# Performance work log

Hardware: AMD Instinct MI355X
Metric: run time of the kernel (lower is better)

The kernel has to match this reference:

```python
import jax, jax.numpy as jnp
import numpy as np

SCALE, K, RADIUS = 4, 32, 0.1
EPS = 1e-5


def fps(p, npoint):
    # Furthest point sampling (CUDA-compatible: starts at index 0). p: (B,N,3) -> (B,npoint) int32
    B, N, _ = p.shape
    d0 = jnp.sum((p - p[:, :1]) ** 2, axis=-1)  # squared dist to point 0, (B,N)

    def step(dist, _):
        nxt = jnp.argmax(dist, axis=-1)                      # (B,)
        lp = p[jnp.arange(B), nxt]                           # (B,3)
        dist = jnp.minimum(dist, jnp.sum((p - lp[:, None]) ** 2, axis=-1))
        return dist, nxt.astype(jnp.int32)

    _, rest = jax.lax.scan(step, d0, None, length=npoint - 1)  # (npoint-1, B)
    idx = jnp.concatenate([jnp.zeros((1, B), jnp.int32), rest], axis=0)
    return idx.T


def ball_query(center, points, radius, k):
    # First-k-by-index neighbors within radius (CUDA ball_query semantics; slots beyond count filled with first hit).
    # center: (B,S,3), points: (B,N,3) -> (B,S,k) int32
    d2 = (jnp.sum(center ** 2, -1)[..., None] + jnp.sum(points ** 2, -1)[:, None, :]
          - 2.0 * jnp.einsum('bsd,bnd->bsn', center, points))  # (B,S,N)
    mask = d2 < radius * radius
    N = points.shape[1]
    score = jnp.where(mask, -jnp.arange(N, dtype=jnp.float32), -jnp.inf)
    vals, idx = jax.lax.top_k(score, k)                      # picks smallest masked indices first
    valid = jnp.isfinite(vals)
    return jnp.where(valid, idx, idx[..., :1])


def convblock(x, w, b, norm=True, act=True):
    # 1x1 conv2d (pointwise) + optional InstanceNorm2d (no affine) + optional ReLU; x: (B,C,S,K)
    x = jnp.einsum('oc,bcsk->bosk', w, x) + b[None, :, None, None]
    if norm:
        m = jnp.mean(x, axis=(2, 3), keepdims=True)
        v = jnp.var(x, axis=(2, 3), keepdims=True)
        x = (x - m) * jax.lax.rsqrt(v + EPS)
    if act:
        x = jax.nn.relu(x)
    return x


def forward(p, f, params):
    B, N, _ = p.shape
    outs_p, outs_f = [p], [f]
    for (w1a, b1a, w1b, b1b, w2a, b2a, w2b, b2b) in params:
        cur_p, cur_f = outs_p[-1], outs_f[-1]
        N = N // SCALE
        idx = fps(cur_p, N)                                          # (B,S)
        center_p = jnp.take_along_axis(cur_p, idx[..., None], axis=1)    # (B,S,3)
        center_f = jnp.take_along_axis(cur_f, idx[:, None, :], axis=2)   # (B,C,S)
        nbr = ball_query(center_p, cur_p, RADIUS, K)                 # (B,S,K)
        gp = jax.vmap(lambda x, i: x[i])(cur_p, nbr)                 # (B,S,K,3)
        dp = jnp.transpose(gp - center_p[:, :, None], (0, 3, 1, 2))  # relative xyz, (B,3,S,K)
        fj = jax.vmap(lambda x, i: x[:, i])(cur_f, nbr)              # (B,C,S,K)
        df = fj - center_f[..., None]                                # 'dp_df' aggregation
        x = jnp.concatenate([dp, df], axis=1)                        # (B,C+3,S,K)
        x = convblock(x, w1a, b1a, norm=True, act=True)
        x = convblock(x, w1b, b1b, norm=False, act=False)
        pooled = jnp.max(x, axis=-1, keepdims=True)
        x = jnp.concatenate([jnp.broadcast_to(pooled, x.shape), x], axis=1)  # (B,2e,S,K)
        x = convblock(x, w2a, b2a, norm=True, act=True)
        x = convblock(x, w2b, b2b, norm=True, act=True)
        outs_f.append(jnp.max(x, axis=-1))                           # (B,e,S)
        outs_p.append(center_p)
    return outs_p, outs_f


def setup_inputs() -> dict:
    key = jax.random.key(0)
    ks = jax.random.split(key, 20)
    B, N = 4, 8192

    def w(k, o, i):
        return jax.random.normal(k, (o, i), jnp.float32) * 0.02

    d = {
        'p': jax.random.uniform(ks[0], (B, N, 3), jnp.float32),
        'f': jax.random.normal(ks[1], (B, 3, N), jnp.float32),
        # stage 1: e=192, c_in=3 -> dp_df channels 6
        'w1_1a': w(ks[2], 192, 6),    'b1_1a': jnp.zeros((192,), jnp.float32),
        'w1_1b': w(ks[3], 192, 192),  'b1_1b': jnp.zeros((192,), jnp.float32),
        'w1_2a': w(ks[4], 384, 384),  'b1_2a': jnp.zeros((384,), jnp.float32),
        'w1_2b': w(ks[5], 192, 384),  'b1_2b': jnp.zeros((192,), jnp.float32),
        # stage 2: e=384, c_in=192 -> dp_df channels 195
        'w2_1a': w(ks[6], 384, 195),  'b2_1a': jnp.zeros((384,), jnp.float32),
        'w2_1b': w(ks[7], 384, 384),  'b2_1b': jnp.zeros((384,), jnp.float32),
        'w2_2a': w(ks[8], 768, 768),  'b2_2a': jnp.zeros((768,), jnp.float32),
        'w2_2b': w(ks[9], 384, 768),  'b2_2b': jnp.zeros((384,), jnp.float32),
    }
    return d


def reference(p, f, w1_1a, b1_1a, w1_1b, b1_1b, w1_2a, b1_2a, w1_2b, b1_2b,
              w2_1a, b2_1a, w2_1b, b2_1b, w2_2a, b2_2a, w2_2b, b2_2b):
    params = [
        (w1_1a, b1_1a, w1_1b, b1_1b, w1_2a, b1_2a, w1_2b, b1_2b),
        (w2_1a, b2_1a, w2_1b, b2_1b, w2_2a, b2_2a, w2_2b, b2_2b),
    ]
    outs_p, outs_f = forward(p, f, params)
    # out_p / out_f lists (excluding the raw inputs, which are passed through unchanged)
    return (outs_p[1], outs_f[1], outs_p[2], outs_f[2])
```

## Files before the change

### kernel.cpp

```cpp
#include <hip/hip_runtime.h>
#include <hip/hip_bf16.h>
#include <hip/hip_fp16.h>
#include <stdint.h>

#define K_NBR 32
#define EPS_F 1e-5f

typedef _Float16 half8v __attribute__((ext_vector_type(8)));
typedef _Float16 half4v __attribute__((ext_vector_type(4)));
typedef float float4v __attribute__((ext_vector_type(4)));

template<int PPT, int MINW>
__global__ __launch_bounds__(256, MINW) void fps_kernel(const float* __restrict__ p, int N, int S,
                                                        int* __restrict__ idx_out,
                                                        float* __restrict__ centers) {
    constexpr int CH = PPT / 4;
    const int b = blockIdx.x;
    const int tid = threadIdx.x;
    const float* pb = p + (size_t)b * N * 3;

    float px[PPT], py[PPT], pz[PPT], dist[PPT];
    const float l0x = pb[0], l0y = pb[1], l0z = pb[2];
#pragma unroll
    for (int j = 0; j < PPT; ++j) {
        int i = j * 256 + tid;
        px[j] = pb[(size_t)i * 3 + 0];
        py[j] = pb[(size_t)i * 3 + 1];
        pz[j] = pb[(size_t)i * 3 + 2];
        float dx = __fsub_rn(px[j], l0x);
        float dy = __fsub_rn(py[j], l0y);
        float dz = __fsub_rn(pz[j], l0z);
        dist[j] = __fadd_rn(__fadd_rn(__fmul_rn(dx, dx), __fmul_rn(dy, dy)), __fmul_rn(dz, dz));
    }

    __shared__ float s_val[2][4];
    __shared__ int   s_idx[2][4];

    if (tid == 0) {
        idx_out[(size_t)b * S] = 0;
        centers[((size_t)b * S) * 3 + 0] = l0x;
        centers[((size_t)b * S) * 3 + 1] = l0y;
        centers[((size_t)b * S) * 3 + 2] = l0z;
    }

    for (int t = 1; t < S; ++t) {
        const int pp = t & 1;
        float v[4]; int ix[4];
#pragma unroll
        for (int k = 0; k < 4; ++k) {
            v[k] = dist[k * CH]; ix[k] = (k * CH) * 256 + tid;
#pragma unroll
            for (int j = 1; j < CH; ++j) {
                if (dist[k * CH + j] > v[k]) { v[k] = dist[k * CH + j]; ix[k] = (k * CH + j) * 256 + tid; }
            }
        }
        float bv = v[0]; int bi = ix[0];
#pragma unroll
        for (int k = 1; k < 4; ++k) if (v[k] > bv) { bv = v[k]; bi = ix[k]; }
#pragma unroll
        for (int off = 32; off >= 1; off >>= 1) {
            float ov = __shfl_down(bv, off);
            int   oi = __shfl_down(bi, off);
            if (ov > bv || (ov == bv && oi < bi)) { bv = ov; bi = oi; }
        }
        if ((tid & 63) == 0) { s_val[pp][tid >> 6] = bv; s_idx[pp][tid >> 6] = bi; }
        __syncthreads();
        bv = s_val[pp][0]; bi = s_idx[pp][0];
#pragma unroll
        for (int w = 1; w < 4; ++w)
            if (s_val[pp][w] > bv || (s_val[pp][w] == bv && s_idx[pp][w] < bi)) { bv = s_val[pp][w]; bi = s_idx[pp][w]; }
        const float lx = pb[(size_t)bi * 3 + 0];
        const float ly = pb[(size_t)bi * 3 + 1];
        const float lz = pb[(size_t)bi * 3 + 2];
        if (tid == 0) {
            idx_out[(size_t)b * S + t] = bi;
            centers[((size_t)b * S + t) * 3 + 0] = lx;
            centers[((size_t)b * S + t) * 3 + 1] = ly;
            centers[((size_t)b * S + t) * 3 + 2] = lz;
        }
#pragma unroll
        for (int j = 0; j < PPT; ++j) {
            float dx = __fsub_rn(px[j], lx);
            float dy = __fsub_rn(py[j], ly);
            float dz = __fsub_rn(pz[j], lz);
            float nd = __fadd_rn(__fadd_rn(__fmul_rn(dx, dx), __fmul_rn(dy, dy)), __fmul_rn(dz, dz));
            dist[j] = fminf(dist[j], nd);
        }
    }
}

__global__ __launch_bounds__(256) void ball_query_kernel(const float* __restrict__ pts,
                                                         const float* __restrict__ ctr,
                                                         int N, int S, int* __restrict__ nbr) {
    int gw   = (int)((blockIdx.x * 256 + threadIdx.x) >> 6);
    int lane = threadIdx.x & 63;
    int b = gw / S;
    int s = gw - b * S;
    const float* pb = pts + (size_t)b * N * 3;
    const float c0 = ctr[((size_t)b * S + s) * 3 + 0];
    const float c1 = ctr[((size_t)b * S + s) * 3 + 1];
    const float c2 = ctr[((size_t)b * S + s) * 3 + 2];
    const float cn = __fadd_rn(__fadd_rn(__fmul_rn(c0, c0), __fmul_rn(c2, c2)), __fmul_rn(c1, c1));
    const float R2 = (float)(0.1 * 0.1);
    int* out = nbr + (size_t)gw * K_NBR;

    int cnt = 0;
    int firstIdx = 0;
    bool haveFirst = false;
    for (int base = 0; base < N && cnt < K_NBR; base += 64) {
        int i = base + lane;
        float x = pb[(size_t)i * 3 + 0];
        float y = pb[(size_t)i * 3 + 1];
        float z = pb[(size_t)i * 3 + 2];
        float pn = __fadd_rn(__fadd_rn(__fmul_rn(x, x), __fmul_rn(z, z)), __fmul_rn(y, y));
        float pr0 = __fmul_rn(c0, x);
        float pr1 = __fmul_rn(c1, y);
        float pr2 = __fmul_rn(c2, z);
        float dt  = __fadd_rn(__fadd_rn(pr0, pr2), pr1);
        float d2 = __fsub_rn(__fadd_rn(cn, pn), __fmul_rn(2.0f, dt));
        bool inR = d2 < R2;
        unsigned long long mask = __ballot(inR);
        if (mask) {
            if (!haveFirst) { haveFirst = true; firstIdx = base + __builtin_ctzll(mask); }
            int rank = __popcll(mask & ((1ull << lane) - 1ull));
            if (inR) {
                int slot = cnt + rank;
                if (slot < K_NBR) out[slot] = i;
            }
            cnt += (int)__popcll(mask);
        }
    }
    if (cnt < K_NBR) {
        for (int sl = cnt + lane; sl < K_NBR; sl += 64) out[sl] = firstIdx;
    }
}

__global__ void gather_cf_kernel(const float* __restrict__ f_b, const int* __restrict__ idx_b,
                                 int N, int S, float* __restrict__ cf, int total) {
    int i = blockIdx.x * 256 + threadIdx.x;
    if (i >= total) return;
    int s = i % S;
    int c = i / S;
    cf[i] = f_b[(size_t)c * N + idx_b[s]];
}

__global__ void build_x_kernel(const float* __restrict__ p_b, const float* __restrict__ f_b,
                               const float* __restrict__ ctr_b, const float* __restrict__ cf,
                               const int* __restrict__ nbr_b,
                               int N, int S, int C, int Cin_pad, int M,
                               _Float16* __restrict__ x) {
    int m = blockIdx.x * 256 + threadIdx.x;
    if (m >= M) return;
    int s = m / K_NBR;
    int n = nbr_b[m];
    const float* pp = p_b + (size_t)n * 3;
    const float* cc = ctr_b + (size_t)s * 3;
    _Float16* row = x + (size_t)m * Cin_pad;
    row[0] = (_Float16)__fsub_rn(pp[0], cc[0]);
    row[1] = (_Float16)__fsub_rn(pp[1], cc[1]);
    row[2] = (_Float16)__fsub_rn(pp[2], cc[2]);
    for (int c = 0; c < C; ++c)
        row[3 + c] = (_Float16)__fsub_rn(f_b[(size_t)c * N + n], cf[(size_t)c * S + s]);
    for (int c = 3 + C; c < Cin_pad; ++c) row[c] = (_Float16)0.f;
}

__global__ void gather_cf2_kernel(const _Float16* __restrict__ ftr, const int* __restrict__ idx_b,
                                  int C, int S, _Float16* __restrict__ cfh, int total) {
    int i = blockIdx.x * 256 + threadIdx.x;
    if (i >= total) return;
    int c = i % C;
    int s = i / C;
    cfh[i] = ftr[(size_t)idx_b[s] * C + c];
}

__global__ void build_x2_kernel(const float* __restrict__ p_b, const _Float16* __restrict__ ftr,
                                const float* __restrict__ ctr_b, const _Float16* __restrict__ cfh,
                                const int* __restrict__ nbr_b,
                                int S, int C, int Cin_pad, int M,
                                _Float16* __restrict__ x) {
    int m = blockIdx.x * 256 + threadIdx.x;
    if (m >= M) return;
    int s = m / K_NBR;
    int n = nbr_b[m];
    const float* pp = p_b + (size_t)n * 3;
    const float* cc = ctr_b + (size_t)s * 3;
    _Float16* row = x + (size_t)m * Cin_pad;
    row[0] = (_Float16)__fsub_rn(pp[0], cc[0]);
    row[1] = (_Float16)__fsub_rn(pp[1], cc[1]);
    row[2] = (_Float16)__fsub_rn(pp[2], cc[2]);
    const _Float16* fr = ftr + (size_t)n * C;
    const _Float16* cr = cfh + (size_t)s * C;
    for (int c = 0; c < C; ++c)
        row[3 + c] = (_Float16)__fsub_rn((float)fr[c], (float)cr[c]);
    for (int c = 3 + C; c < Cin_pad; ++c) row[c] = (_Float16)0.f;
}

__global__ void wconv_kernel(const float* __restrict__ W, int Cin, int Cin_pad,
                             _Float16* __restrict__ Wh, int total) {
    int i = blockIdx.x * 256 + threadIdx.x;
    if (i >= total) return;
    int o = i / Cin_pad, c = i - o * Cin_pad;
    Wh[i] = (c < Cin) ? (_Float16)W[(size_t)o * Cin + c] : (_Float16)0.f;
}

template<bool HAS_POOL, bool NORM_IN, bool STATS>
__global__ __launch_bounds__(256) void conv_mfma_kernel(
    const _Float16* __restrict__ Wh, const float* __restrict__ bias,
    int Cin_pad, int C1,
    const _Float16* __restrict__ Xp,
    const _Float16* __restrict__ X,
    const float* __restrict__ muIn, const float* __restrict__ riIn,
    _Float16* __restrict__ Y,
    int M, int Cout,
    float* __restrict__ psum, float* __restrict__ psq) {
    const int wave = threadIdx.x >> 6;
    const int lane = threadIdx.x & 63;
    const int row  = lane & 15;
    const int kg   = lane >> 4;
    const int m0   = blockIdx.x * 128 + wave * 32;
    const int o0   = blockIdx.y * 64;
    const int mIdx0 = m0 + row;
    const int mIdx1 = m0 + 16 + row;

    float4v acc[2][4];
#pragma unroll
    for (int t = 0; t < 4; ++t) {
        const float* bp = bias + o0 + 16 * t + kg * 4;
        float4v bv4 = (float4v){bp[0], bp[1], bp[2], bp[3]};
        acc[0][t] = bv4;
        acc[1][t] = bv4;
    }
    const int C2 = Cin_pad - C1;
    if (HAS_POOL) {
        const _Float16* pr0 = Xp + (size_t)(mIdx0 >> 5) * C1;
        const _Float16* pr1 = Xp + (size_t)(mIdx1 >> 5) * C1;
        for (int c0 = 0; c0 < C1; c0 += 32) {
            half8v b0 = *(const half8v*)(pr0 + c0 + kg * 8);
            half8v b1 = *(const half8v*)(pr1 + c0 + kg * 8);
#pragma unroll
            for (int t = 0; t < 4; ++t) {
                half8v afr = *(const half8v*)(Wh + (size_t)(o0 + 16 * t + row) * Cin_pad + c0 + kg * 8);
                acc[0][t] = __builtin_amdgcn_mfma_f32_16x16x32_f16(afr, b0, acc[0][t], 0, 0, 0);
                acc[1][t] = __builtin_amdgcn_mfma_f32_16x16x32_f16(afr, b1, acc[1][t], 0, 0, 0);
            }
        }
    }
    const _Float16* xr0 = X + (size_t)mIdx0 * C2;
    const _Float16* xr1 = X + (size_t)mIdx1 * C2;
    for (int c0 = 0; c0 < C2; c0 += 32) {
        half8v b0 = *(const half8v*)(xr0 + c0 + kg * 8);
        half8v b1 = *(const half8v*)(xr1 + c0 + kg * 8);
        if (NORM_IN) {
            const int cb = c0 + kg * 8;
#pragma unroll
            for (int r = 0; r < 8; ++r) {
                float mu = muIn[cb + r], ri = riIn[cb + r];
                b0[r] = (_Float16)fmaxf(((float)b0[r] - mu) * ri, 0.f);
                b1[r] = (_Float16)fmaxf(((float)b1[r] - mu) * ri, 0.f);
            }
        }
#pragma unroll
        for (int t = 0; t < 4; ++t) {
            half8v afr = *(const half8v*)(Wh + (size_t)(o0 + 16 * t + row) * Cin_pad + C1 + c0 + kg * 8);
            acc[0][t] = __builtin_amdgcn_mfma_f32_16x16x32_f16(afr, b0, acc[0][t], 0, 0, 0);
            acc[1][t] = __builtin_amdgcn_mfma_f32_16x16x32_f16(afr, b1, acc[1][t], 0, 0, 0);
        }
    }
#pragma unroll
    for (int w = 0; w < 2; ++w) {
        int mi = (w == 0) ? mIdx0 : mIdx1;
#pragma unroll
        for (int t = 0; t < 4; ++t) {
            half4v hv;
            hv[0] = (_Float16)acc[w][t][0];
            hv[1] = (_Float16)acc[w][t][1];
            hv[2] = (_Float16)acc[w][t][2];
            hv[3] = (_Float16)acc[w][t][3];
            *(half4v*)(Y + (size_t)mi * Cout + o0 + 16 * t + kg * 4) = hv;
        }
    }
    if (STATS) {
        float s[16], q[16];
#pragma unroll
        for (int t = 0; t < 4; ++t)
#pragma unroll
            for (int r = 0; r < 4; ++r) {
                float a0 = acc[0][t][r], a1 = acc[1][t][r];
                s[t * 4 + r] = a0 + a1;
                q[t * 4 + r] = fmaf(a0, a0, a1 * a1);
            }
#pragma unroll
        for (int mask = 1; mask <= 8; mask <<= 1) {
#pragma unroll
            for (int i = 0; i < 16; ++i) {
                s[i] += __shfl_xor(s[i], mask);
                q[i] += __shfl_xor(q[i], mask);
            }
        }
        if (row == 0) {
            int mrow = blockIdx.x * 4 + wave;
            float* ps = psum + (size_t)mrow * Cout + o0;
            float* pq = psq  + (size_t)mrow * Cout + o0;
#pragma unroll
            for (int t = 0; t < 4; ++t)
#pragma unroll
                for (int r = 0; r < 4; ++r) {
                    ps[16 * t + kg * 4 + r] = s[t * 4 + r];
                    pq[16 * t + kg * 4 + r] = q[t * 4 + r];
                }
        }
    }
}

__global__ __launch_bounds__(256) void in_fin_kernel(const float* __restrict__ psum,
                                                     const float* __restrict__ psq,
                                                     int C, int rows, int M,
                                                     float* __restrict__ mean,
                                                     float* __restrict__ rinv) {
    int c = blockIdx.x;
    int tid = threadIdx.x;
    float s = 0.f, q = 0.f;
    for (int r = tid; r < rows; r += 256) {
        s += psum[(size_t)r * C + c];
        q += psq [(size_t)r * C + c];
    }
#pragma unroll
    for (int off = 32; off >= 1; off >>= 1) {
        s += __shfl_down(s, off);
        q += __shfl_down(q, off);
    }
    __shared__ float sS[4], sQ[4];
    if ((tid & 63) == 0) { sS[tid >> 6] = s; sQ[tid >> 6] = q; }
    __syncthreads();
    if (tid == 0) {
        float fs = sS[0] + sS[1] + sS[2] + sS[3];
        float fq = sQ[0] + sQ[1] + sQ[2] + sQ[3];
        float mu  = fs / (float)M;
        float var = fq / (float)M - mu * mu;
        mean[c] = mu;
        rinv[c] = rsqrtf(fmaxf(var, 0.f) + EPS_F);
    }
}

__global__ void maxk_kernel(const _Float16* __restrict__ Y, int C,
                            _Float16* __restrict__ pooled, int total) {
    int i = blockIdx.x * 256 + threadIdx.x;
    if (i >= total) return;
    int c = i % C;
    int s = i / C;
    const _Float16* base = Y + (size_t)s * 32 * C + c;
    float mx = (float)base[0];
#pragma unroll 8
    for (int k = 1; k < K_NBR; ++k) mx = fmaxf(mx, (float)base[(size_t)k * C]);
    pooled[(size_t)s * C + c] = (_Float16)mx;
}

__global__ void maxk_out_in_kernel(const _Float16* __restrict__ Y, int C, int S,
                                   const float* __restrict__ mean, const float* __restrict__ rinv,
                                   float* __restrict__ outf_b, _Float16* __restrict__ ftr_out,
                                   int total) {
    int i = blockIdx.x * 256 + threadIdx.x;
    if (i >= total) return;
    int o = i % C;
    int s = i / C;
    const _Float16* base = Y + (size_t)s * 32 * C + o;
    float mx = (float)base[0];
#pragma unroll 8
    for (int k = 1; k < K_NBR; ++k) mx = fmaxf(mx, (float)base[(size_t)k * C]);
    float val = fmaxf((mx - mean[o]) * rinv[o], 0.f);
    outf_b[(size_t)o * S + s] = val;
    if (ftr_out) ftr_out[i] = (_Float16)val;
}

struct StageArgs {
    const float *P, *F, *CTR;
    const _Float16* FTR;
    const int *NBR, *IDX;
    int N, S, C, e, Cin_pad;
    const _Float16 *Wa1, *Wb1, *Wa2, *Wb2;
    const float *ba1, *bb1, *ba2, *bb2;
    float* OUTF;
    _Float16* FTR_OUT;
};

static void run_conv_stage(const StageArgs& a, hipStream_t stream,
                           uint8_t* R1, uint8_t* R2, size_t xo_off,
                           _Float16* pooled, float* cf_ws, _Float16* cfh_ws,
                           float* psum, float* psq, float* mean_ws, float* rinv_ws) {
    const int M = a.S * K_NBR;
    const int e = a.e;
    const int srows = M / 32;
    _Float16* x0 = (_Float16*)R1;
    _Float16* RA = (_Float16*)(R1 + xo_off);
    _Float16* RC = (_Float16*)R1;
    _Float16* RB = (_Float16*)R2;
    _Float16* RD = (_Float16*)R2;
    for (int b = 0; b < 4; ++b) {
        const float* p_b   = a.P + (size_t)b * a.N * 3;
        const float* ctr_b = a.CTR + (size_t)b * a.S * 3;
        const int*   nbr_b = a.NBR + (size_t)b * a.S * K_NBR;
        const int*   idx_b = a.IDX + (size_t)b * a.S;
        float*       outf_b= a.OUTF + (size_t)b * e * a.S;

        if (a.FTR == nullptr) {
            const float* f_b = a.F + (size_t)b * a.C * a.N;
            gather_cf_kernel<<<(a.C * a.S + 255) / 256, 256, 0, stream>>>(f_b, idx_b, a.N, a.S, cf_ws, a.C * a.S);
            build_x_kernel<<<M / 256, 256, 0, stream>>>(p_b, f_b, ctr_b, cf_ws, nbr_b,
                                                        a.N, a.S, a.C, a.Cin_pad, M, x0);
        } else {
            const _Float16* ftr_b = a.FTR + (size_t)b * a.N * a.C;
            gather_cf2_kernel<<<(a.C * a.S + 255) / 256, 256, 0, stream>>>(ftr_b, idx_b, a.C, a.S, cfh_ws, a.C * a.S);
            build_x2_kernel<<<M / 256, 256, 0, stream>>>(p_b, ftr_b, ctr_b, cfh_ws, nbr_b,
                                                         a.S, a.C, a.Cin_pad, M, x0);
        }

        conv_mfma_kernel<false, false, true><<<dim3(M / 128, e / 64), 256, 0, stream>>>(
            a.Wa1, a.ba1, a.Cin_pad, 0, nullptr, x0, nullptr, nullptr, RA, M, e, psum, psq);
        in_fin_kernel<<<e, 256, 0, stream>>>(psum, psq, e, srows, M, mean_ws, rinv_ws);
        conv_mfma_kernel<false, true, false><<<dim3(M / 128, e / 64), 256, 0, stream>>>(
            a.Wb1, a.bb1, e, 0, nullptr, RA, mean_ws, rinv_ws, RB, M, e, nullptr, nullptr);
        maxk_kernel<<<(e * (M / 32) + 255) / 256, 256, 0, stream>>>(RB, e, pooled, e * (M / 32));
        conv_mfma_kernel<true, false, true><<<dim3(M / 128, (2 * e) / 64), 256, 0, stream>>>(
            a.Wa2, a.ba2, 2 * e, e, pooled, RB, nullptr, nullptr, RC, M, 2 * e, psum, psq);
        in_fin_kernel<<<2 * e, 256, 0, stream>>>(psum, psq, 2 * e, srows, M, mean_ws, rinv_ws);
        conv_mfma_kernel<false, true, true><<<dim3(M / 128, e / 64), 256, 0, stream>>>(
            a.Wb2, a.bb2, 2 * e, 0, nullptr, RC, mean_ws, rinv_ws, RD, M, e, psum, psq);
        in_fin_kernel<<<e, 256, 0, stream>>>(psum, psq, e, srows, M, mean_ws, rinv_ws);
        _Float16* ftr_b_out = a.FTR_OUT ? a.FTR_OUT + (size_t)b * a.S * e : nullptr;
        maxk_out_in_kernel<<<(e * a.S + 255) / 256, 256, 0, stream>>>(RD, e, a.S, mean_ws, rinv_ws,
                                                                      outf_b, ftr_b_out, e * a.S);
    }
}

extern "C" void kernel_launch(void* const* d_in, const int* in_sizes, int n_in,
                              void* d_out, int out_size, void* d_ws, size_t ws_size,
                              hipStream_t stream) {
    const float* p    = (const float*)d_in[0];
    const float* f    = (const float*)d_in[1];
    const float* w1a1 = (const float*)d_in[2];
    const float* b1a1 = (const float*)d_in[3];
    const float* w1b1 = (const float*)d_in[4];
    const float* b1b1 = (const float*)d_in[5];
    const float* w1a2 = (const float*)d_in[6];
    const float* b1a2 = (const float*)d_in[7];
    const float* w1b2 = (const float*)d_in[8];
    const float* b1b2 = (const float*)d_in[9];
    const float* w2a1 = (const float*)d_in[10];
    const float* b2a1 = (const float*)d_in[11];
    const float* w2b1 = (const float*)d_in[12];
    const float* b2b1 = (const float*)d_in[13];
    const float* w2a2 = (const float*)d_in[14];
    const float* b2a2 = (const float*)d_in[15];
    const float* w2b2 = (const float*)d_in[16];
    const float* b2b2 = (const float*)d_in[17];

    float* out   = (float*)d_out;
    float* outp1 = out;
    float* outf1 = out + 24576;
    float* outp2 = outf1 + 1572864;
    float* outf2 = outp2 + 6144;

    uint8_t* wsp = (uint8_t*)d_ws;
    uint8_t* wend = wsp + ws_size;
    auto alloc = [&](size_t bytes) -> void* {
        void* r = wsp;
        wsp += (bytes + 255) & ~(size_t)255;
        return r;
    };
    int*   idx1   = (int*)  alloc((size_t)4 * 2048 * 4);
    int*   idx2   = (int*)  alloc((size_t)4 * 512 * 4);
    int*   nbr1   = (int*)  alloc((size_t)4 * 2048 * K_NBR * 4);
    int*   nbr2   = (int*)  alloc((size_t)4 * 512 * K_NBR * 4);
    float* cf_ws  = (float*)alloc((size_t)192 * 512 * 4);
    _Float16* cfh_ws = (_Float16*)alloc((size_t)512 * 192 * 2);
    float* mean_ws= (float*)alloc((size_t)768 * 4);
    float* rinv_ws= (float*)alloc((size_t)768 * 4);
    float* psum   = (float*)alloc((size_t)2048 * 768 * 4);
    float* psq    = (float*)alloc((size_t)2048 * 768 * 4);
    _Float16* pooled = (_Float16*)alloc((size_t)2048 * 384 * 2);
    _Float16* ftr1   = (_Float16*)alloc((size_t)4 * 2048 * 192 * 2);
    _Float16* h1a1 = (_Float16*)alloc((size_t)192 * 32  * 2);
    _Float16* h1b1 = (_Float16*)alloc((size_t)192 * 192 * 2);
    _Float16* h1a2 = (_Float16*)alloc((size_t)384 * 384 * 2);
    _Float16* h1b2 = (_Float16*)alloc((size_t)192 * 384 * 2);
    _Float16* h2a1 = (_Float16*)alloc((size_t)384 * 224 * 2);
    _Float16* h2b1 = (_Float16*)alloc((size_t)384 * 384 * 2);
    _Float16* h2a2 = (_Float16*)alloc((size_t)768 * 768 * 2);
    _Float16* h2b2 = (_Float16*)alloc((size_t)384 * 768 * 2);
    if (wsp > wend) return;

    auto wc = [&](const float* W, int Cin, int Cpad, int Cout, _Float16* Wh) {
        int tot = Cout * Cpad;
        wconv_kernel<<<(tot + 255) / 256, 256, 0, stream>>>(W, Cin, Cpad, Wh, tot);
    };
    wc(w1a1, 6,   32,  192, h1a1);
    wc(w1b1, 192, 192, 192, h1b1);
    wc(w1a2, 384, 384, 384, h1a2);
    wc(w1b2, 384, 384, 192, h1b2);
    wc(w2a1, 195, 224, 384, h2a1);
    wc(w2b1, 384, 384, 384, h2b1);
    wc(w2a2, 768, 768, 768, h2a2);
    wc(w2b2, 768, 768, 384, h2b2);

    fps_kernel<32, 1><<<4, 256, 0, stream>>>(p, 8192, 2048, idx1, outp1);
    ball_query_kernel<<<(4 * 2048) / 4, 256, 0, stream>>>(p, outp1, 8192, 2048, nbr1);
    fps_kernel<8, 2><<<4, 256, 0, stream>>>(outp1, 2048, 512, idx2, outp2);
    ball_query_kernel<<<(4 * 512) / 4, 256, 0, stream>>>(outp1, outp2, 2048, 512, nbr2);

    const size_t MB = (size_t)1024 * 1024;
    uint8_t* R1 = (uint8_t*)alloc(48 * MB);
    uint8_t* R2 = (uint8_t*)alloc(24 * MB);
    if (wsp > wend) return;

    StageArgs s1 { p, f, outp1, nullptr, nbr1, idx1, 8192, 2048, 3, 192, 32,
                   h1a1, h1b1, h1a2, h1b2, b1a1, b1b1, b1a2, b1b2, outf1, ftr1 };
    StageArgs s2 { outp1, nullptr, outp2, ftr1, nbr2, idx2, 2048, 512, 192, 384, 224,
                   h2a1, h2b1, h2a2, h2b2, b2a1, b2b1, b2a2, b2b2, outf2, nullptr };

    run_conv_stage(s1, stream, R1, R2, 8 * MB, pooled, cf_ws, cfh_ws, psum, psq, mean_ws, rinv_ws);
    run_conv_stage(s2, stream, R1, R2, 8 * MB, pooled, cf_ws, cfh_ws, psum, psq, mean_ws, rinv_ws);
}
```

Baseline: 5.916 ms.

## Cache FPS points in LDS, fuse argmax into update, batch index writes

The FPS kernel now stages all points in shared memory, so the winning point's coordinates are read from LDS instead of global memory on the serial critical path. The per-thread argmax is folded into the distance update loop. Output index and center writes are buffered in shared memory and flushed once every 256 iterations by all threads, rather than written by thread 0 on every step. This adds shared memory use, about 100KB for the large instantiation, and an extra barrier on flush iterations. The launch-bounds occupancy hint for the second FPS instantiation also drops from 2 to 1.

```diff
diff --git a/kernel.cpp b/kernel.cpp
--- a/kernel.cpp
+++ b/kernel.cpp
@@ -15,11 +15,19 @@
                                                         int* __restrict__ idx_out,
                                                         float* __restrict__ centers) {
     constexpr int CH = PPT / 4;
+    constexpr int NPT = PPT * 256;
     const int b = blockIdx.x;
     const int tid = threadIdx.x;
     const float* pb = p + (size_t)b * N * 3;
 
+    __shared__ float m_x[NPT], m_y[NPT], m_z[NPT];
+    __shared__ float s_val[2][4];
+    __shared__ int   s_idx[2][4];
+    __shared__ int   r_i[256];
+    __shared__ float r_x[256], r_y[256], r_z[256];
+
     float px[PPT], py[PPT], pz[PPT], dist[PPT];
+    float v[4]; int ixl[4];
     const float l0x = pb[0], l0y = pb[1], l0z = pb[2];
 #pragma unroll
     for (int j = 0; j < PPT; ++j) {
@@ -27,14 +35,16 @@
         px[j] = pb[(size_t)i * 3 + 0];
         py[j] = pb[(size_t)i * 3 + 1];
         pz[j] = pb[(size_t)i * 3 + 2];
+        m_x[i] = px[j]; m_y[i] = py[j]; m_z[i] = pz[j];
         float dx = __fsub_rn(px[j], l0x);
         float dy = __fsub_rn(py[j], l0y);
         float dz = __fsub_rn(pz[j], l0z);
         dist[j] = __fadd_rn(__fadd_rn(__fmul_rn(dx, dx), __fmul_rn(dy, dy)), __fmul_rn(dz, dz));
-    }
-
-    __shared__ float s_val[2][4];
-    __shared__ int   s_idx[2][4];
+        constexpr int KJ0 = 0;  (void)KJ0;
+        int k = j / CH;
+        if ((j % CH) == 0) { v[k] = dist[j]; ixl[k] = j * 256 + tid; }
+        else if (dist[j] > v[k]) { v[k] = dist[j]; ixl[k] = j * 256 + tid; }
+    }
 
     if (tid == 0) {
         idx_out[(size_t)b * S] = 0;
@@ -42,21 +52,13 @@
         centers[((size_t)b * S) * 3 + 1] = l0y;
         centers[((size_t)b * S) * 3 + 2] = l0z;
     }
+    __syncthreads();
 
     for (int t = 1; t < S; ++t) {
         const int pp = t & 1;
-        float v[4]; int ix[4];
-#pragma unroll
-        for (int k = 0; k < 4; ++k) {
-            v[k] = dist[k * CH]; ix[k] = (k * CH) * 256 + tid;
-#pragma unroll
-            for (int j = 1; j < CH; ++j) {
-                if (dist[k * CH + j] > v[k]) { v[k] = dist[k * CH + j]; ix[k] = (k * CH + j) * 256 + tid; }
-            }
-        }
-        float bv = v[0]; int bi = ix[0];
-#pragma unroll
-        for (int k = 1; k < 4; ++k) if (v[k] > bv) { bv = v[k]; bi = ix[k]; }
+        float bv = v[0]; int bi = ixl[0];
+#pragma unroll
+        for (int k = 1; k < 4; ++k) if (v[k] > bv) { bv = v[k]; bi = ixl[k]; }
 #pragma unroll
         for (int off = 32; off >= 1; off >>= 1) {
             float ov = __shfl_down(bv, off);
@@ -65,18 +67,26 @@
         }
         if ((tid & 63) == 0) { s_val[pp][tid >> 6] = bv; s_idx[pp][tid >> 6] = bi; }
         __syncthreads();
+        if ((t & 255) == 0) {
+            int s0 = (t - 256) + tid;
+            if (s0 >= 1) {
+                idx_out[(size_t)b * S + s0] = r_i[tid];
+                centers[((size_t)b * S + s0) * 3 + 0] = r_x[tid];
+                centers[((size_t)b * S + s0) * 3 + 1] = r_y[tid];
+                centers[((size_t)b * S + s0) * 3 + 2] = r_z[tid];
+            }
+            __syncthreads();
+        }
         bv = s_val[pp][0]; bi = s_idx[pp][0];
 #pragma unroll
         for (int w = 1; w < 4; ++w)
             if (s_val[pp][w] > bv || (s_val[pp][w] == bv && s_idx[pp][w] < bi)) { bv = s_val[pp][w]; bi = s_idx[pp][w]; }
-        const float lx = pb[(size_t)bi * 3 + 0];
-        const float ly = pb[(size_t)bi * 3 + 1];
-        const float lz = pb[(size_t)bi * 3 + 2];
+        const float lx = m_x[bi];
+        const float ly = m_y[bi];
+        const float lz = m_z[bi];
         if (tid == 0) {
-            idx_out[(size_t)b * S + t] = bi;
-            centers[((size_t)b * S + t) * 3 + 0] = lx;
-            centers[((size_t)b * S + t) * 3 + 1] = ly;
-            centers[((size_t)b * S + t) * 3 + 2] = lz;
+            r_i[t & 255] = bi;
+            r_x[t & 255] = lx; r_y[t & 255] = ly; r_z[t & 255] = lz;
         }
 #pragma unroll
         for (int j = 0; j < PPT; ++j) {
@@ -85,6 +95,20 @@
             float dz = __fsub_rn(pz[j], lz);
             float nd = __fadd_rn(__fadd_rn(__fmul_rn(dx, dx), __fmul_rn(dy, dy)), __fmul_rn(dz, dz));
             dist[j] = fminf(dist[j], nd);
+            int k = j / CH;
+            if ((j % CH) == 0) { v[k] = dist[j]; ixl[k] = j * 256 + tid; }
+            else if (dist[j] > v[k]) { v[k] = dist[j]; ixl[k] = j * 256 + tid; }
+        }
+    }
+    __syncthreads();
+    {
+        int base = (S - 1) & ~255;
+        int s0 = base + tid;
+        if (s0 >= 1 && s0 <= S - 1) {
+            idx_out[(size_t)b * S + s0] = r_i[tid];
+            centers[((size_t)b * S + s0) * 3 + 0] = r_x[tid];
+            centers[((size_t)b * S + s0) * 3 + 1] = r_y[tid];
+            centers[((size_t)b * S + s0) * 3 + 2] = r_z[tid];
         }
     }
 }
@@ -504,7 +528,7 @@
 
     fps_kernel<32, 1><<<4, 256, 0, stream>>>(p, 8192, 2048, idx1, outp1);
     ball_query_kernel<<<(4 * 2048) / 4, 256, 0, stream>>>(p, outp1, 8192, 2048, nbr1);
-    fps_kernel<8, 2><<<4, 256, 0, stream>>>(outp1, 2048, 512, idx2, outp2);
+    fps_kernel<8, 1><<<4, 256, 0, stream>>>(outp1, 2048, 512, idx2, outp2);
     ball_query_kernel<<<(4 * 512) / 4, 256, 0, stream>>>(outp1, outp2, 2048, 512, nbr2);
 
     const size_t MB = (size_t)1024 * 1024;
```

Result: faster. 5.725 ms (-3.2%).
